# Optimization experiments

Hardware: AMD Instinct MI355X
Metric: run time of the kernel (lower is better)

## Reference

```python
import jax, jax.numpy as jnp
import numpy as np

N, E, F, T = 10000, 160000, 4, 12   # nodes, edges, features, periods
C, HID, OUT = 512, 256, 12          # tgcn out_channels, head hidden, output_dim


def setup_inputs() -> dict:
    key = jax.random.key(0)
    ks = jax.random.split(key, 24)
    g = lambda k, s: (jax.random.normal(k, s, dtype=jnp.float32) * 0.05)
    inp = {
        "x": jax.random.normal(ks[0], (N, F, T), dtype=jnp.float32),
        "edge_index": jax.random.randint(ks[1], (2, E), 0, N, dtype=jnp.int32),
        "edge_attr": jax.random.uniform(ks[2], (E,), dtype=jnp.float32),
        "att": g(ks[3], (T,)),
        # TGCN gates: GCNConv (W [F,C], b [C]) + Linear on cat([conv, H]) ([2C,C], [C])
        "Wz_g": g(ks[4], (F, C)), "bz_g": jnp.zeros((C,), jnp.float32),
        "Wz_l": g(ks[5], (2 * C, C)), "bz_l": jnp.zeros((C,), jnp.float32),
        "Wr_g": g(ks[6], (F, C)), "br_g": jnp.zeros((C,), jnp.float32),
        "Wr_l": g(ks[7], (2 * C, C)), "br_l": jnp.zeros((C,), jnp.float32),
        "Wh_g": g(ks[8], (F, C)), "bh_g": jnp.zeros((C,), jnp.float32),
        "Wh_l": g(ks[9], (2 * C, C)), "bh_l": jnp.zeros((C,), jnp.float32),
        # dense head
        "W1": g(ks[10], (C, HID)), "b1": jnp.zeros((HID,), jnp.float32),
        "W2": g(ks[11], (HID, OUT)), "b2": jnp.zeros((OUT,), jnp.float32),
    }
    return inp


def reference(x, edge_index, edge_attr, att,
              Wz_g, bz_g, Wz_l, bz_l,
              Wr_g, br_g, Wr_l, br_l,
              Wh_g, bh_g, Wh_l, bh_l,
              W1, b1, W2, b2):
    n = x.shape[0]
    # GCN normalization with self loops (fill value 1.0), computed once
    loops = jnp.arange(n, dtype=edge_index.dtype)
    src = jnp.concatenate([edge_index[0], loops])
    dst = jnp.concatenate([edge_index[1], loops])
    w = jnp.concatenate([edge_attr, jnp.ones((n,), x.dtype)])
    deg = jax.ops.segment_sum(w, dst, num_segments=n)
    dinv = jax.lax.rsqrt(jnp.maximum(deg, 1e-12))
    norm = dinv[src] * w * dinv[dst]  # [E+N]

    def gcn(xt, W, b):
        xw = xt @ W                                   # [N,C]
        msg = norm[:, None] * xw[src]                 # gather over edges
        return jax.ops.segment_sum(msg, dst, num_segments=n) + b

    probs = jax.nn.softmax(att)            # attention over periods
    xt_seq = jnp.moveaxis(x, -1, 0)        # [T,N,F]
    H0 = jnp.zeros((n, C), x.dtype)

    def step(carry, inp):
        H, acc = carry
        xt, p = inp
        z = jax.nn.sigmoid(jnp.concatenate([gcn(xt, Wz_g, bz_g), H], axis=1) @ Wz_l + bz_l)
        r = jax.nn.sigmoid(jnp.concatenate([gcn(xt, Wr_g, br_g), H], axis=1) @ Wr_l + br_l)
        ht = jnp.tanh(jnp.concatenate([gcn(xt, Wh_g, bh_g), H * r], axis=1) @ Wh_l + bh_l)
        Hn = z * H + (1.0 - z) * ht
        return (Hn, acc + p * Hn), None

    (Hf, H_accum), _ = jax.lax.scan(step, (H0, H0), (xt_seq, probs))
    out_hidden = H_accum
    h = jax.nn.relu(H_accum)
    h = jax.nn.relu(h @ W1 + b1)
    h = h @ W2 + b2
    return (h, out_hidden)
```

## Files before the change

### kernel.cpp

```cpp
#include <hip/hip_runtime.h>
#include <math.h>

#define NF 48
#define TT 12

typedef __bf16 v8bf __attribute__((ext_vector_type(8)));
typedef float v16f __attribute__((ext_vector_type(16)));


__global__ void k_init(float* __restrict__ deg, int* __restrict__ cnt, int n) {
  int i = blockIdx.x * blockDim.x + threadIdx.x;
  if (i < n) { deg[i] = 1.0f; cnt[i] = 0; cnt[n + i] = 0; }
}

__global__ void k_edge(const int* __restrict__ dst, const float* __restrict__ w,
                       float* __restrict__ deg, int* __restrict__ cnt, int e) {
  int i = blockIdx.x * blockDim.x + threadIdx.x;
  if (i < e) {
    int d = dst[i];
    atomicAdd(&deg[d], w[i]);
    atomicAdd(&cnt[d], 1);
  }
}


__global__ void k_scan1(const int* __restrict__ cnt, int* __restrict__ pscan,
                        int* __restrict__ bsum, const float* __restrict__ deg,
                        float* __restrict__ dinv, int n) {
  __shared__ int s[256];
  int i = blockIdx.x * 256 + threadIdx.x;
  int v = (i < n) ? cnt[i] : 0;
  s[threadIdx.x] = v;
  __syncthreads();
  for (int off = 1; off < 256; off <<= 1) {
    int t = 0;
    if (threadIdx.x >= off) t = s[threadIdx.x - off];
    __syncthreads();
    s[threadIdx.x] += t;
    __syncthreads();
  }
  if (i < n) {
    pscan[i] = s[threadIdx.x] - v;
    dinv[i] = rsqrtf(fmaxf(deg[i], 1e-12f));
  }
  if (threadIdx.x == 255) bsum[blockIdx.x] = s[255];
}

__global__ void k_scan2(const int* __restrict__ bsum, int* __restrict__ bpre, int nb,
                        const float* __restrict__ att, float* __restrict__ probs) {
  if (blockIdx.x == 0 && threadIdx.x == 0) {
    int run = 0;
    for (int b = 0; b < nb; b++) { bpre[b] = run; run += bsum[b]; }
  }
  if (blockIdx.x == 0 && threadIdx.x == 64) {
    float m = -1e30f;
    for (int t = 0; t < TT; t++) m = fmaxf(m, att[t]);
    float e[TT], s = 0.f;
    for (int t = 0; t < TT; t++) { e[t] = expf(att[t] - m); s += e[t]; }
    for (int t = 0; t < TT; t++) probs[t] = e[t] / s;
  }
}

__global__ void k_scan3(const int* __restrict__ pscan, const int* __restrict__ bpre,
                        int* __restrict__ offs, int n, int e) {
  int i = blockIdx.x * blockDim.x + threadIdx.x;
  if (i < n) offs[i] = pscan[i] + bpre[i >> 8];
  if (i == 0) offs[n] = e;
}

__global__ void k_place(const int* __restrict__ src, const int* __restrict__ dst,
                        const float* __restrict__ w, const int* __restrict__ offs,
                        int* __restrict__ fill, int* __restrict__ csrc,
                        float* __restrict__ cw, int e) {
  int i = blockIdx.x * blockDim.x + threadIdx.x;
  if (i >= e) return;
  int d = dst[i];
  int p = offs[d] + atomicAdd(&fill[d], 1);
  csrc[p] = src[i];
  cw[p] = w[i];
}

__global__ void k_gather(const int* __restrict__ offs, const int* __restrict__ csrc,
                         const float* __restrict__ cw, const float* __restrict__ dinv,
                         const float* __restrict__ x, float* __restrict__ Y, int n) {
  int tg = blockIdx.x * blockDim.x + threadIdx.x;
  if (tg >= n * 12) return;
  int i = tg / 12, q = tg % 12;
  float di = dinv[i];
  const float4* x4 = (const float4*)x;
  float4 sv = x4[(size_t)i * 12 + q];
  float ax = di * sv.x, ay = di * sv.y, az = di * sv.z, aw = di * sv.w;
  int e1 = offs[i + 1];
  for (int e = offs[i]; e < e1; e++) {
    int s = csrc[e];
    float wv = cw[e] * dinv[s];
    float4 xv = x4[(size_t)s * 12 + q];
    ax = fmaf(wv, xv.x, ax); ay = fmaf(wv, xv.y, ay);
    az = fmaf(wv, xv.z, az); aw = fmaf(wv, xv.w, aw);
  }
  float4 o = make_float4(di * ax, di * ay, di * az, di * aw);
  ((float4*)Y)[(size_t)i * 12 + q] = o;
}

__device__ __forceinline__ size_t packIdx128(int n, int k) {
  int row = n & 127;
  int c = (k & 31) >> 3;
  return (size_t)(n >> 7) * (128 * 512) + (size_t)(k >> 5) * (128 * 32) +
         (size_t)row * 32 + (size_t)((c ^ (row & 3)) << 3) + (k & 7);
}

__global__ void k_pack3(const float* __restrict__ Wzl, const float* __restrict__ Wrl,
                        const float* __restrict__ Whl, const float* __restrict__ W1,
                        __bf16* __restrict__ WzrP, __bf16* __restrict__ WhP,
                        __bf16* __restrict__ W1P) {
  __shared__ __bf16 t[64][72];
  int modew = blockIdx.z;
  if (modew == 1 && blockIdx.x >= 8) return;
  if (modew == 2 && blockIdx.x >= 4) return;
  int n0 = blockIdx.x * 64, k0 = blockIdx.y * 64;
  __bf16* WT = (modew == 0) ? WzrP : (modew == 1) ? WhP : W1P;
#pragma unroll
  for (int p = 0; p < 4; p++) {
    int kk = p * 16 + (threadIdx.x >> 4);
    int nn = (threadIdx.x & 15) * 4;
    int n = n0 + nn, k = k0 + kk;
    float4 v;
    if (modew == 2) {
      v = *(const float4*)(W1 + (size_t)k * 256 + n);
    } else {
      const float* src = (modew == 1) ? Whl : Wzl;
      int nc = n;
      if (modew == 0 && n >= 512) { src = Wrl; nc = n - 512; }
      v = *(const float4*)(src + (size_t)(512 + k) * 512 + nc);
    }
    t[kk][nn + 0] = (__bf16)v.x; t[kk][nn + 1] = (__bf16)v.y;
    t[kk][nn + 2] = (__bf16)v.z; t[kk][nn + 3] = (__bf16)v.w;
  }
  __syncthreads();
#pragma unroll
  for (int u = 0; u < 2; u++) {
    int unit = threadIdx.x * 2 + u;
    int nl = unit >> 3, kg = unit & 7;
    v8bf o;
#pragma unroll
    for (int j = 0; j < 8; j++) o[j] = t[kg * 8 + j][nl];
    *(v8bf*)(WT + packIdx128(n0 + nl, k0 + kg * 8)) = o;
  }
}

__global__ void k_build_eff3(const float* __restrict__ Wzg, const float* __restrict__ Wzl,
                             const float* __restrict__ bzg, const float* __restrict__ bzl,
                             const float* __restrict__ Wrg, const float* __restrict__ Wrl,
                             const float* __restrict__ brg, const float* __restrict__ brl,
                             const float* __restrict__ Whg, const float* __restrict__ Whl,
                             const float* __restrict__ bhg, const float* __restrict__ bhl,
                             float* __restrict__ WzrE, float* __restrict__ bzrE,
                             float* __restrict__ WhE, float* __restrict__ bhE) {
  int idx = blockIdx.x * blockDim.x + threadIdx.x;
  if (idx >= 3 * 5 * 512) return;
  int seg = idx / 2560;
  int r = (idx % 2560) / 512, c = idx % 512;
  const float *Wg, *Wl, *bg, *bl;
  float *We, *be;
  int ostride, ooff;
  if (seg == 0) { Wg = Wzg; Wl = Wzl; bg = bzg; bl = bzl; We = WzrE; be = bzrE; ostride = 1024; ooff = 0; }
  else if (seg == 1) { Wg = Wrg; Wl = Wrl; bg = brg; bl = brl; We = WzrE; be = bzrE; ostride = 1024; ooff = 512; }
  else { Wg = Whg; Wl = Whl; bg = bhg; bl = bhl; We = WhE; be = bhE; ostride = 512; ooff = 0; }
  float s = 0.f;
  if (r < 4) {
    for (int k = 0; k < 512; k++) s += Wg[r * 512 + k] * Wl[k * 512 + c];
    We[r * ostride + ooff + c] = s;
  } else {
    for (int k = 0; k < 512; k++) s += bg[k] * Wl[k * 512 + c];
    be[ooff + c] = s + bl[c];
  }
}

__global__ void k_wy3(const float* __restrict__ WzrE, const float* __restrict__ bzrE,
                      const float* __restrict__ WhE, const float* __restrict__ bhE,
                      const float* __restrict__ b1,
                      __bf16* __restrict__ WyZR, __bf16* __restrict__ WyH,
                      __bf16* __restrict__ Wy1) {
  int idx = blockIdx.x * blockDim.x + threadIdx.x;
  const float* Weff; const float* beff; __bf16* out; int Nout, loc;
  if (idx < 1024 * 16) { Weff = WzrE; beff = bzrE; out = WyZR; Nout = 1024; loc = idx; }
  else if (idx < (1024 + 512) * 16) { Weff = WhE; beff = bhE; out = WyH; Nout = 512; loc = idx - 1024 * 16; }
  else if (idx < (1024 + 512 + 256) * 16) { Weff = nullptr; beff = b1; out = Wy1; Nout = 256; loc = idx - (1024 + 512) * 16; }
  else return;
  int n = loc >> 4, k = loc & 15;
  float v = 0.f;
  if (k < 4) v = Weff ? Weff[k * Nout + n] : 0.f;
  else if (k == 4) v = beff[n];
  out[(size_t)(n >> 7) * 2048 + (size_t)(n & 127) * 16 + k] = (__bf16)v;
}

__global__ void k_yat0(const float* __restrict__ Y,
                       const float* __restrict__ WzrE, const float* __restrict__ bzrE,
                       const float* __restrict__ WhE, const float* __restrict__ bhE,
                       __bf16* __restrict__ Ya, __bf16* __restrict__ H1, int n) {
  int idx = blockIdx.x * blockDim.x + threadIdx.x;
  int nt0 = n * 512;
  if (idx < nt0) {
    int i = idx >> 9, c = idx & 511;
    float y0 = Y[(size_t)i * NF + 0], y1 = Y[(size_t)i * NF + 12];
    float y2 = Y[(size_t)i * NF + 24], y3 = Y[(size_t)i * NF + 36];
    float pz = bzrE[c] + y0 * WzrE[c] + y1 * WzrE[1024 + c] +
               y2 * WzrE[2048 + c] + y3 * WzrE[3072 + c];
    float ph = bhE[c] + y0 * WhE[c] + y1 * WhE[512 + c] +
               y2 * WhE[1024 + c] + y3 * WhE[1536 + c];
    float z = 1.f / (1.f + expf(-pz));
    H1[idx] = (__bf16)((1.f - z) * tanhf(ph));
  } else {
    int r = idx - nt0;
    if (r >= TT * n * 16) return;
    int t = r / (n * 16);
    int loc = r % (n * 16);
    int nn = loc >> 4, k = loc & 15;
    float v = 0.f;
    if (k < 4) v = Y[(size_t)nn * NF + k * TT + t];
    else if (k == 4) v = 1.f;
    Ya[r] = (__bf16)v;
  }
}

template <int MODE>
__global__ __launch_bounds__(256, 6) void k_mm(
    const __bf16* __restrict__ Abf, const __bf16* __restrict__ Bp,
    const __bf16* __restrict__ Rbf, const __bf16* __restrict__ Zbf,
    const __bf16* __restrict__ Ay, const __bf16* __restrict__ Wy,
    float* __restrict__ Ofp, __bf16* __restrict__ Obf, __bf16* __restrict__ ObfR,
    int M, int RB) {
  constexpr int CB = (MODE == 0) ? 8 : (MODE == 1) ? 4 : 2;
  constexpr int BUFS = 6144;
  __shared__ __bf16 smem[12288];

  int s = blockIdx.x;
  int grp = 8 * CB;
  int local = s % grp;
  int rowblk = (s / grp) * 8 + (local & 7);
  int colblk = local >> 3;
  if (rowblk >= RB) return;
  const int row0 = rowblk * 64;

  const int tid = threadIdx.x;
  const int lane = tid & 63, w = tid >> 6;
  const int wr = (w >> 1) * 32, wc = (w & 1) * 64;
  const int l31 = lane & 31, lh = lane >> 5;

  const int ar = tid >> 2, ac = tid & 3;
  const __bf16* At = Abf + (size_t)(row0 + ar) * 512 + ac * 8;
  const __bf16* Rt = Rbf + (size_t)(row0 + ar) * 512 + ac * 8;
  const __bf16* Bt = Bp + (size_t)colblk * (128 * 512);
  const int aoff = ar * 32 + ((ac ^ (ar & 3)) << 3);

  v16f acc[2];
#pragma unroll
  for (int j = 0; j < 2; j++)
#pragma unroll
    for (int q = 0; q < 16; q++) acc[j][q] = 0.f;

  uint4 ra, rr, rb0, rb1;
  rr = make_uint4(0, 0, 0, 0);

  auto gload = [&](int kt) {
    ra = *(const uint4*)(At + kt * 32);
    if constexpr (MODE == 1) rr = *(const uint4*)(Rt + kt * 32);
    rb0 = *(const uint4*)(Bt + (size_t)kt * 4096 + (size_t)tid * 8);
    rb1 = *(const uint4*)(Bt + (size_t)kt * 4096 + (size_t)(256 + tid) * 8);
  };
  auto gloadY = [&]() {
    if (tid < 128)
      ra = *(const uint4*)(Ay + (size_t)(row0 + (tid >> 1)) * 16 + (tid & 1) * 8);
    rb0 = *(const uint4*)(Wy + (size_t)colblk * 2048 + (size_t)(tid >> 1) * 16 + (tid & 1) * 8);
  };
  auto lstore = [&](int buf) {
    __bf16* base = smem + buf * BUFS;
    if constexpr (MODE == 1) {
      v8bf h = *(const v8bf*)&ra;
      v8bf r = *(const v8bf*)&rr;
      v8bf o;
#pragma unroll
      for (int q = 0; q < 8; q++) o[q] = (__bf16)((float)h[q] * (float)r[q]);
      *(v8bf*)&base[aoff] = o;
    } else {
      *(uint4*)&base[aoff] = ra;
    }
    *(uint4*)&base[2048 + (size_t)tid * 8] = rb0;
    *(uint4*)&base[2048 + (size_t)(256 + tid) * 8] = rb1;
  };
  auto lstoreY = [&](int buf) {
    __bf16* base = smem + buf * BUFS;
    if (tid < 128) *(uint4*)&base[(tid >> 1) * 16 + (tid & 1) * 8] = ra;
    *(uint4*)&base[2048 + (size_t)(tid >> 1) * 16 + (tid & 1) * 8] = rb0;
  };
  auto compute = [&](int buf) {
    const __bf16* base = smem + buf * BUFS;
#pragma unroll
    for (int ks = 0; ks < 2; ks++) {
      int kc = ks * 2 + lh;
      int fr = wr + l31;
      v8bf a = *(const v8bf*)&base[fr * 32 + ((kc ^ (fr & 3)) << 3)];
#pragma unroll
      for (int ni = 0; ni < 2; ni++) {
        int fc = wc + ni * 32 + l31;
        v8bf b = *(const v8bf*)&base[2048 + fc * 32 + ((kc ^ (fc & 3)) << 3)];
        acc[ni] = __builtin_amdgcn_mfma_f32_32x32x16_bf16(a, b, acc[ni], 0, 0, 0);
      }
    }
  };
  auto computeY = [&](int buf) {
    const __bf16* base = smem + buf * BUFS;
    v8bf a = *(const v8bf*)&base[(wr + l31) * 16 + lh * 8];
#pragma unroll
    for (int ni = 0; ni < 2; ni++) {
      v8bf b = *(const v8bf*)&base[2048 + (wc + ni * 32 + l31) * 16 + lh * 8];
      acc[ni] = __builtin_amdgcn_mfma_f32_32x32x16_bf16(a, b, acc[ni], 0, 0, 0);
    }
  };

  gload(0);
  lstore(0);
  gload(1);
  __syncthreads();
#pragma unroll
  for (int kt = 0; kt <= 16; kt++) {
    if (kt < 16) {
      if (kt < 15) lstore((kt + 1) & 1);
      else lstoreY((kt + 1) & 1);
      if (kt < 14) gload(kt + 2);
      else if (kt == 14) gloadY();
      compute(kt & 1);
      __syncthreads();
    } else {
      computeY(kt & 1);
    }
  }
  __syncthreads();

  if constexpr (MODE == 2) {
#pragma unroll
    for (int ni = 0; ni < 2; ni++) {
      int cl = wc + ni * 32 + l31;
#pragma unroll
      for (int reg = 0; reg < 16; reg++) {
        int rg = row0 + wr + (reg & 3) + ((reg >> 2) << 3) + (lh << 2);
        if (rg >= M) continue;
        Ofp[(size_t)rg * 256 + colblk * 128 + cl] = fmaxf(acc[ni][reg], 0.f);
      }
    }
  } else if constexpr (MODE == 0) {
#pragma unroll
    for (int ni = 0; ni < 2; ni++) {
      int cl = wc + ni * 32 + l31;
#pragma unroll
      for (int reg = 0; reg < 16; reg++) {
        int lr = wr + (reg & 3) + ((reg >> 2) << 3) + (lh << 2);
        smem[lr * 128 + cl] = (__bf16)(1.f / (1.f + expf(-acc[ni][reg])));
      }
    }
    __syncthreads();
    int row = tid >> 2, seg = (tid & 3) * 32;
    int rg = row0 + row;
    if (rg < M) {
      __bf16* dst = (colblk < 4) ? Obf : ObfR;
      int cof = (colblk & 3) * 128;
#pragma unroll
      for (int q = 0; q < 4; q++) {
        uint4 v = *(const uint4*)&smem[row * 128 + seg + q * 8];
        *(uint4*)(dst + (size_t)rg * 512 + cof + seg + q * 8) = v;
      }
    }
  } else {
    float* sF = (float*)smem;
#pragma unroll
    for (int h = 0; h < 2; h++) {
      if ((w >> 1) == h) {
#pragma unroll
        for (int ni = 0; ni < 2; ni++) {
          int cl = wc + ni * 32 + l31;
#pragma unroll
          for (int reg = 0; reg < 16; reg++) {
            int lr = (reg & 3) + ((reg >> 2) << 3) + (lh << 2);
            sF[lr * 128 + cl] = tanhf(acc[ni][reg]);
          }
        }
      }
      __syncthreads();
      int row = tid >> 3, seg = (tid & 7) * 16;
      int rg = row0 + h * 32 + row;
      if (rg < M) {
        int cg0 = colblk * 128 + seg;
#pragma unroll
        for (int q = 0; q < 2; q++) {
          v8bf z8 = *(const v8bf*)(Zbf + (size_t)rg * 512 + cg0 + q * 8);
          v8bf h8 = *(const v8bf*)(Abf + (size_t)rg * 512 + cg0 + q * 8);
          v8bf o;
#pragma unroll
          for (int j = 0; j < 8; j++) {
            float z = (float)z8[j];
            float ht = sF[row * 128 + seg + q * 8 + j];
            o[j] = (__bf16)(z * (float)h8[j] + (1.f - z) * ht);
          }
          *(v8bf*)(Obf + (size_t)rg * 512 + cg0 + q * 8) = o;
        }
      }
      if (h == 0) __syncthreads();
    }
  }
}

__global__ void k_acc(const __bf16* __restrict__ hist, const float* __restrict__ probs,
                      float* __restrict__ acc, __bf16* __restrict__ accRelu, int n) {
  int idx = blockIdx.x * blockDim.x + threadIdx.x;
  if (idx >= n * 64) return;
  size_t off = (size_t)idx * 8;
  size_t S = (size_t)n * 512;
  float s[8] = {0, 0, 0, 0, 0, 0, 0, 0};
#pragma unroll
  for (int t = 0; t < TT; t++) {
    float p = probs[t];
    v8bf h = *(const v8bf*)(hist + (size_t)(t + 1) * S + off);
#pragma unroll
    for (int j = 0; j < 8; j++) s[j] = fmaf(p, (float)h[j], s[j]);
  }
  *(float4*)(acc + off) = make_float4(s[0], s[1], s[2], s[3]);
  *(float4*)(acc + off + 4) = make_float4(s[4], s[5], s[6], s[7]);
  v8bf rl;
#pragma unroll
  for (int j = 0; j < 8; j++) rl[j] = (__bf16)fmaxf(s[j], 0.f);
  *(v8bf*)(accRelu + off) = rl;
}

__global__ void k_head2(const float* __restrict__ T1, const float* __restrict__ W2,
                        const float* __restrict__ b2, float* __restrict__ out0, int M) {
  int idx = blockIdx.x * blockDim.x + threadIdx.x;
  if (idx >= M * 12) return;
  int i = idx / 12, c = idx % 12;
  const float* tr = T1 + (size_t)i * 256;
  float s = b2[c];
  for (int k = 0; k < 256; k++) s = fmaf(tr[k], W2[k * 12 + c], s);
  out0[idx] = s;
}


extern "C" void kernel_launch(void* const* d_in, const int* in_sizes, int n_in,
                              void* d_out, int out_size, void* d_ws, size_t ws_size,
                              hipStream_t stream) {
  const float* x   = (const float*)d_in[0];
  const int*   ei  = (const int*)d_in[1];
  const float* ea  = (const float*)d_in[2];
  const float* att = (const float*)d_in[3];
  const float* Wzg = (const float*)d_in[4];  const float* bzg = (const float*)d_in[5];
  const float* Wzl = (const float*)d_in[6];  const float* bzl = (const float*)d_in[7];
  const float* Wrg = (const float*)d_in[8];  const float* brg = (const float*)d_in[9];
  const float* Wrl = (const float*)d_in[10]; const float* brl = (const float*)d_in[11];
  const float* Whg = (const float*)d_in[12]; const float* bhg = (const float*)d_in[13];
  const float* Whl = (const float*)d_in[14]; const float* bhl = (const float*)d_in[15];
  const float* W1  = (const float*)d_in[16]; const float* b1  = (const float*)d_in[17];
  const float* W2  = (const float*)d_in[18]; const float* b2  = (const float*)d_in[19];

  const int N = in_sizes[0] / NF;
  const int E = in_sizes[1] / 2;
  const int* srcI = ei;
  const int* dstI = ei + E;

  float* out0 = (float*)d_out;
  float* accO = (float*)d_out + (size_t)N * 12;

  char* wp = (char*)d_ws;
  auto carve = [&](size_t bytes) -> void* {
    void* p = (void*)wp;
    wp += (bytes + 255) & ~(size_t)255;
    return p;
  };
  float*  deg     = (float*)carve((size_t)N * 4);
  float*  dinv    = (float*)carve((size_t)N * 4);
  float*  probs   = (float*)carve(64);
  float*  Y       = (float*)carve((size_t)N * NF * 4);
  __bf16* WzrP    = (__bf16*)carve((size_t)1024 * 512 * 2);
  __bf16* WhP     = (__bf16*)carve((size_t)512 * 512 * 2);
  __bf16* W1P     = (__bf16*)carve((size_t)256 * 512 * 2);
  float*  Wzr_eff = (float*)carve((size_t)4 * 1024 * 4);
  float*  bzr_eff = (float*)carve((size_t)1024 * 4);
  float*  Wh_eff  = (float*)carve((size_t)4 * 512 * 4);
  float*  bh_eff  = (float*)carve((size_t)512 * 4);
  __bf16* hist    = (__bf16*)carve((size_t)(TT + 1) * N * 512 * 2);
  __bf16* Zbf     = (__bf16*)carve((size_t)N * 512 * 2);
  __bf16* Rbf     = (__bf16*)carve((size_t)N * 512 * 2);
  __bf16* accRelu = (__bf16*)carve((size_t)N * 512 * 2);
  float*  T1      = (float*)carve((size_t)N * 256 * 4);
  __bf16* Ya      = (__bf16*)carve((size_t)TT * N * 16 * 2);
  __bf16* WyZR    = (__bf16*)carve((size_t)1024 * 16 * 2);
  __bf16* WyH     = (__bf16*)carve((size_t)512 * 16 * 2);
  __bf16* Wy1     = (__bf16*)carve((size_t)256 * 16 * 2);
  int*    cnt     = (int*)carve((size_t)2 * N * 4);
  int*    fill    = cnt + N;
  int*    offs    = (int*)carve((size_t)(N + 1) * 4);
  int*    pscan   = (int*)carve((size_t)N * 4);
  int*    bsum    = (int*)carve(256);
  int*    bpre    = (int*)carve(256);
  int*    csrc    = (int*)carve((size_t)E * 4);
  float*  cw      = (float*)carve((size_t)E * 4);
  (void)carve(512 * 1024);
  (void)ws_size; (void)n_in; (void)out_size;

  const int TPB = 256;
  auto cdiv = [](int a, int b) { return (a + b - 1) / b; };
  const size_t S = (size_t)N * 512;

  k_init<<<cdiv(N, TPB), TPB, 0, stream>>>(deg, cnt, N);
  k_edge<<<cdiv(E, TPB), TPB, 0, stream>>>(dstI, ea, deg, cnt, E);

  const int nb = cdiv(N, 256);
  k_scan1<<<nb, 256, 0, stream>>>(cnt, pscan, bsum, deg, dinv, N);
  k_scan2<<<1, 128, 0, stream>>>(bsum, bpre, nb, att, probs);
  k_scan3<<<cdiv(N, TPB), TPB, 0, stream>>>(pscan, bpre, offs, N, E);
  k_place<<<cdiv(E, TPB), TPB, 0, stream>>>(srcI, dstI, ea, offs, fill, csrc, cw, E);
  k_gather<<<cdiv(N * 12, TPB), TPB, 0, stream>>>(offs, csrc, cw, dinv, x, Y, N);

  {
    dim3 gp(16, 8, 3);
    k_pack3<<<gp, 256, 0, stream>>>(Wzl, Wrl, Whl, W1, WzrP, WhP, W1P);
  }
  k_build_eff3<<<cdiv(3 * 5 * 512, TPB), TPB, 0, stream>>>(
      Wzg, Wzl, bzg, bzl, Wrg, Wrl, brg, brl, Whg, Whl, bhg, bhl,
      Wzr_eff, bzr_eff, Wh_eff, bh_eff);
  k_wy3<<<cdiv((1024 + 512 + 256) * 16, TPB), TPB, 0, stream>>>(
      Wzr_eff, bzr_eff, Wh_eff, bh_eff, b1, WyZR, WyH, Wy1);

  k_yat0<<<cdiv(N * 512 + TT * N * 16, TPB), TPB, 0, stream>>>(
      Y, Wzr_eff, bzr_eff, Wh_eff, bh_eff, Ya, hist + S, N);

  const int RB = cdiv(N, 64);
  const int nGrp = cdiv(RB, 8);
  for (int t = 1; t < TT; t++) {
    const __bf16* Hbt = hist + (size_t)t * S;
    __bf16* Hbn = hist + (size_t)(t + 1) * S;
    const __bf16* Yat = Ya + (size_t)t * N * 16;
    k_mm<0><<<64 * nGrp, 256, 0, stream>>>(Hbt, WzrP, nullptr, nullptr, Yat, WyZR,
                                           nullptr, Zbf, Rbf, N, RB);
    k_mm<1><<<32 * nGrp, 256, 0, stream>>>(Hbt, WhP, Rbf, Zbf, Yat, WyH,
                                           nullptr, Hbn, nullptr, N, RB);
  }

  k_acc<<<cdiv(N * 64, TPB), TPB, 0, stream>>>(hist, probs, accO, accRelu, N);
  k_mm<2><<<16 * nGrp, 256, 0, stream>>>(accRelu, W1P, nullptr, nullptr, Ya, Wy1,
                                         T1, nullptr, nullptr, N, RB);
  k_head2<<<cdiv(N * 12, TPB), TPB, 0, stream>>>(T1, W2, b2, out0, N);
}
```

Baseline: 801.3 us.

## Stage GEMM tiles via global_load_lds and precompute H*r in gate epilogue

The GEMM kernel now loads A and B tiles straight from global memory into LDS with global_load_lds, replacing the register round trip and separate LDS stores. The swizzle moves to the global address side. The H*r product for the candidate gate is now formed in the z/r kernel's epilogue, which writes r*H, so the h-kernel reads a ready A operand and needs no per-element multiply in its staging path. The aim is lower register pressure and less staging instruction overhead. In exchange, the z/r epilogue does an extra global read of H, and the direct-to-LDS layout has to match the swizzled compute reads.

```diff
diff --git a/kernel.cpp b/kernel.cpp
--- a/kernel.cpp
+++ b/kernel.cpp
@@ -6,6 +6,12 @@
 
 typedef __bf16 v8bf __attribute__((ext_vector_type(8)));
 typedef float v16f __attribute__((ext_vector_type(16)));
+
+__device__ __forceinline__ void gld16(const void* g, void* l) {
+  __builtin_amdgcn_global_load_lds(
+      (const __attribute__((address_space(1))) void*)(uintptr_t)g,
+      (__attribute__((address_space(3))) void*)(uintptr_t)l, 16, 0, 0);
+}
 
 
 __global__ void k_init(float* __restrict__ deg, int* __restrict__ cnt, int n) {
@@ -225,8 +231,8 @@
 
 template <int MODE>
 __global__ __launch_bounds__(256, 6) void k_mm(
-    const __bf16* __restrict__ Abf, const __bf16* __restrict__ Bp,
-    const __bf16* __restrict__ Rbf, const __bf16* __restrict__ Zbf,
+    const __bf16* __restrict__ Agm, const __bf16* __restrict__ Bp,
+    const __bf16* __restrict__ Hc, const __bf16* __restrict__ Zbf,
     const __bf16* __restrict__ Ay, const __bf16* __restrict__ Wy,
     float* __restrict__ Ofp, __bf16* __restrict__ Obf, __bf16* __restrict__ ObfR,
     int M, int RB) {
@@ -248,10 +254,8 @@
   const int l31 = lane & 31, lh = lane >> 5;
 
   const int ar = tid >> 2, ac = tid & 3;
-  const __bf16* At = Abf + (size_t)(row0 + ar) * 512 + ac * 8;
-  const __bf16* Rt = Rbf + (size_t)(row0 + ar) * 512 + ac * 8;
+  const __bf16* At = Agm + (size_t)(row0 + ar) * 512 + ((ac ^ (ar & 3)) << 3);
   const __bf16* Bt = Bp + (size_t)colblk * (128 * 512);
-  const int aoff = ar * 32 + ((ac ^ (ar & 3)) << 3);
 
   v16f acc[2];
 #pragma unroll
@@ -259,39 +263,18 @@
 #pragma unroll
     for (int q = 0; q < 16; q++) acc[j][q] = 0.f;
 
-  uint4 ra, rr, rb0, rb1;
-  rr = make_uint4(0, 0, 0, 0);
-
-  auto gload = [&](int kt) {
-    ra = *(const uint4*)(At + kt * 32);
-    if constexpr (MODE == 1) rr = *(const uint4*)(Rt + kt * 32);
-    rb0 = *(const uint4*)(Bt + (size_t)kt * 4096 + (size_t)tid * 8);
-    rb1 = *(const uint4*)(Bt + (size_t)kt * 4096 + (size_t)(256 + tid) * 8);
+  auto stage = [&](int buf, int kt) {
+    __bf16* base = smem + buf * BUFS;
+    gld16(At + kt * 32, base + w * 512);
+    const __bf16* bs = Bt + (size_t)kt * 4096 + (size_t)tid * 8;
+    gld16(bs, base + 2048 + w * 512);
+    gld16(bs + 2048, base + 4096 + w * 512);
   };
-  auto gloadY = [&]() {
-    if (tid < 128)
-      ra = *(const uint4*)(Ay + (size_t)(row0 + (tid >> 1)) * 16 + (tid & 1) * 8);
-    rb0 = *(const uint4*)(Wy + (size_t)colblk * 2048 + (size_t)(tid >> 1) * 16 + (tid & 1) * 8);
-  };
-  auto lstore = [&](int buf) {
+  auto stageY = [&](int buf) {
     __bf16* base = smem + buf * BUFS;
-    if constexpr (MODE == 1) {
-      v8bf h = *(const v8bf*)&ra;
-      v8bf r = *(const v8bf*)&rr;
-      v8bf o;
-#pragma unroll
-      for (int q = 0; q < 8; q++) o[q] = (__bf16)((float)h[q] * (float)r[q]);
-      *(v8bf*)&base[aoff] = o;
-    } else {
-      *(uint4*)&base[aoff] = ra;
-    }
-    *(uint4*)&base[2048 + (size_t)tid * 8] = rb0;
-    *(uint4*)&base[2048 + (size_t)(256 + tid) * 8] = rb1;
-  };
-  auto lstoreY = [&](int buf) {
-    __bf16* base = smem + buf * BUFS;
-    if (tid < 128) *(uint4*)&base[(tid >> 1) * 16 + (tid & 1) * 8] = ra;
-    *(uint4*)&base[2048 + (size_t)(tid >> 1) * 16 + (tid & 1) * 8] = rb0;
+    if (w < 2)
+      gld16(Ay + (size_t)(row0 + (tid >> 1)) * 16 + (tid & 1) * 8, base + w * 512);
+    gld16(Wy + (size_t)colblk * 2048 + (size_t)tid * 8, base + 2048 + w * 512);
   };
   auto compute = [&](int buf) {
     const __bf16* base = smem + buf * BUFS;
@@ -318,23 +301,17 @@
     }
   };
 
-  gload(0);
-  lstore(0);
-  gload(1);
+  stage(0, 0);
   __syncthreads();
 #pragma unroll
-  for (int kt = 0; kt <= 16; kt++) {
-    if (kt < 16) {
-      if (kt < 15) lstore((kt + 1) & 1);
-      else lstoreY((kt + 1) & 1);
-      if (kt < 14) gload(kt + 2);
-      else if (kt == 14) gloadY();
-      compute(kt & 1);
-      __syncthreads();
-    } else {
-      computeY(kt & 1);
-    }
-  }
+  for (int kt = 0; kt < 16; kt++) {
+    int cur = kt & 1;
+    if (kt < 15) stage(cur ^ 1, kt + 1);
+    else stageY(cur ^ 1);
+    compute(cur);
+    __syncthreads();
+  }
+  computeY(0);
   __syncthreads();
 
   if constexpr (MODE == 2) {
@@ -362,12 +339,23 @@
     int row = tid >> 2, seg = (tid & 3) * 32;
     int rg = row0 + row;
     if (rg < M) {
-      __bf16* dst = (colblk < 4) ? Obf : ObfR;
       int cof = (colblk & 3) * 128;
-#pragma unroll
-      for (int q = 0; q < 4; q++) {
-        uint4 v = *(const uint4*)&smem[row * 128 + seg + q * 8];
-        *(uint4*)(dst + (size_t)rg * 512 + cof + seg + q * 8) = v;
+      if (colblk < 4) {
+#pragma unroll
+        for (int q = 0; q < 4; q++) {
+          uint4 v = *(const uint4*)&smem[row * 128 + seg + q * 8];
+          *(uint4*)(Obf + (size_t)rg * 512 + cof + seg + q * 8) = v;
+        }
+      } else {
+#pragma unroll
+        for (int q = 0; q < 4; q++) {
+          v8bf r8 = *(const v8bf*)&smem[row * 128 + seg + q * 8];
+          v8bf h8 = *(const v8bf*)(Agm + (size_t)rg * 512 + cof + seg + q * 8);
+          v8bf o;
+#pragma unroll
+          for (int j = 0; j < 8; j++) o[j] = (__bf16)((float)r8[j] * (float)h8[j]);
+          *(v8bf*)(ObfR + (size_t)rg * 512 + cof + seg + q * 8) = o;
+        }
       }
     }
   } else {
@@ -393,7 +381,7 @@
 #pragma unroll
         for (int q = 0; q < 2; q++) {
           v8bf z8 = *(const v8bf*)(Zbf + (size_t)rg * 512 + cg0 + q * 8);
-          v8bf h8 = *(const v8bf*)(Abf + (size_t)rg * 512 + cg0 + q * 8);
+          v8bf h8 = *(const v8bf*)(Hc + (size_t)rg * 512 + cg0 + q * 8);
           v8bf o;
 #pragma unroll
           for (int j = 0; j < 8; j++) {
@@ -539,7 +527,7 @@
     const __bf16* Yat = Ya + (size_t)t * N * 16;
     k_mm<0><<<64 * nGrp, 256, 0, stream>>>(Hbt, WzrP, nullptr, nullptr, Yat, WyZR,
                                            nullptr, Zbf, Rbf, N, RB);
-    k_mm<1><<<32 * nGrp, 256, 0, stream>>>(Hbt, WhP, Rbf, Zbf, Yat, WyH,
+    k_mm<1><<<32 * nGrp, 256, 0, stream>>>(Rbf, WhP, Hbt, Zbf, Yat, WyH,
                                            nullptr, Hbn, nullptr, N, RB);
   }
 
```

After: 709.8 us. -11.4%, faster.
